# Optimization experiments

Measured on AMD Instinct MI355X. Metric: run time of the kernel, lower is better.

The kernel has to match this reference:

```python
import jax, jax.numpy as jnp
import numpy as np

DIM = 384; HEADS = 6; K = 10; G = 2
GC = DIM // G            # group channel dim
HD = DIM // HEADS        # head dim
SCALE = HD ** -0.5
LN_EPS = 1e-5


def _sqdist(a, b):
    # a: [..., n, 3], b: [..., m, 3] -> [..., n, m]
    return (jnp.sum(a * a, -1)[..., :, None]
            + jnp.sum(b * b, -1)[..., None, :]
            - 2.0 * jnp.einsum('...nc,...mc->...nm', a, b))


def setup_inputs() -> dict:
    key = jax.random.key(0)
    ks = jax.random.split(key, 12)
    B, N, M = 4, 1024, 1024
    s = 0.02
    return {
        'q': jax.random.normal(ks[0], (B, N, DIM), jnp.float32),
        'q_pos': jax.random.normal(ks[1], (B, N, 3), jnp.float32),
        'v': jax.random.normal(ks[2], (B, M, DIM), jnp.float32),
        'v_pos': jax.random.normal(ks[3], (B, M, 3), jnp.float32),
        'Wq': jax.random.normal(ks[4], (DIM, DIM), jnp.float32) * s,
        'Wk': jax.random.normal(ks[5], (DIM, DIM), jnp.float32) * s,
        'Wv': jax.random.normal(ks[6], (DIM, DIM), jnp.float32) * s,
        'Wvoff': jax.random.normal(ks[7], (DIM, DIM), jnp.float32) * s,
        'Woff1': jax.random.normal(ks[8], (DIM, 2 * GC), jnp.float32) * s,
        'boff1': jnp.zeros((DIM,), jnp.float32),
        'ln_g': jnp.ones((DIM,), jnp.float32),
        'ln_b': jnp.zeros((DIM,), jnp.float32),
        'Woff2': jax.random.normal(ks[9], (3, DIM), jnp.float32) * s,
        'Wproj': jax.random.normal(ks[10], (DIM, DIM), jnp.float32) * s,
        'bproj': jnp.zeros((DIM,), jnp.float32),
    }


def reference(q, q_pos, v, v_pos, Wq, Wk, Wv, Wvoff, Woff1, boff1,
              ln_g, ln_b, Woff2, Wproj, bproj):
    B, N, C = q.shape
    M = v.shape[1]

    # --- knn_point: K nearest v_pos for each q_pos ---
    idx = jax.lax.top_k(-_sqdist(q_pos, v_pos), K)[1]        # [B,N,K]
    idx_flat = idx.reshape(B, N * K, 1)

    qp = q @ Wq.T                                            # [B,N,C]
    v_off = v @ Wvoff.T                                      # [B,M,C]

    # index_points gathers
    local_v = jnp.take_along_axis(v_off, idx_flat, axis=1).reshape(B, N, K, C)
    local_v_pos = jnp.take_along_axis(v_pos, idx_flat, axis=1).reshape(B, N, K, 3)

    # group split: 'b n k (g c) -> b g n k c'
    off_local_v = local_v.reshape(B, N, K, G, GC).transpose(0, 3, 1, 2, 4)  # [B,G,N,K,GC]
    group_q = qp.reshape(B, N, G, GC).transpose(0, 2, 1, 3)                 # [B,G,N,GC]

    shift_feat = jnp.concatenate(
        [off_local_v, jnp.broadcast_to(group_q[:, :, :, None, :], (B, G, N, K, GC))], -1)

    # linear_offset MLP: Linear -> LayerNorm -> GELU(exact) -> Linear, then tanh
    h = shift_feat @ Woff1.T + boff1                          # [B,G,N,K,DIM]
    mu = h.mean(-1, keepdims=True)
    var = h.var(-1, keepdims=True)
    h = (h - mu) / jnp.sqrt(var + LN_EPS) * ln_g + ln_b
    h = jax.nn.gelu(h, approximate=False)
    offset = jnp.tanh(h @ Woff2.T)                            # [B,G,N,K,3]

    shift_pos = (local_v_pos[:, None] + offset).reshape(B, G, N * K, 3)
    vg = v.reshape(B, M, G, GC).transpose(0, 2, 1, 3)         # [B,G,M,GC]

    # --- three_nn + reciprocal-distance three_interpolate ---
    sqd = _sqdist(shift_pos, v_pos[:, None])                  # [B,G,N*K,M]
    negd, idx3 = jax.lax.top_k(-sqd, 3)                       # 3 smallest
    dist = jnp.sqrt(jnp.maximum(-negd, 0.0))                  # [B,G,N*K,3]
    w = 1.0 / (dist + 1e-8)
    w = w / jnp.sum(w, -1, keepdims=True)
    feats = jnp.take_along_axis(vg, idx3.reshape(B, G, N * K * 3, 1), axis=2)
    feats = feats.reshape(B, G, N * K, 3, GC)
    interp = jnp.einsum('bgnj,bgnjc->bgnc', w, feats)         # [B,G,N*K,GC]
    # '(b g) (n k) c -> b n k (g c)'
    interp = interp.reshape(B, G, N, K, GC).transpose(0, 2, 3, 1, 4).reshape(B, N, K, C)

    # --- local cross-attention (each query attends to its K interpolated feats) ---
    kf = (interp @ Wk.T).reshape(B, N, K, HEADS, HD)
    vf = (interp @ Wv.T).reshape(B, N, K, HEADS, HD)
    qh = qp.reshape(B, N, HEADS, HD)
    attn = jnp.einsum('bnhd,bnkhd->bhnk', qh, kf) * SCALE
    attn = jax.nn.softmax(attn, axis=-1)
    out = jnp.einsum('bhnk,bnkhd->bnhd', attn, vf).reshape(B, N, C)
    return out @ Wproj.T + bproj
```

## Files before the change

### kernel.cpp

```cpp
#include <hip/hip_runtime.h>
#include <math.h>

#define NB 4
#define NN 1024
#define NM 1024
#define NC 384
#define NK 10
#define NG 2
#define NGC 192
#define NH 6

#define GSZ ((size_t)NB * NM * NC)
#define QSZ ((size_t)NB * NN * NC)
#define NCNC ((size_t)NC * NC)

#define OFF_WQ 0
#define OFF_W1B 147456
#define OFF_WK0 221184
#define OFF_WK1 294912
#define OFF_WV0 368640
#define OFF_WV1 442368
#define OFF_WPROJ 516096
#define WT_ALL_FLOATS 663552

__device__ __forceinline__ float wred_sum(float v) {
#pragma unroll
  for (int m = 32; m >= 1; m >>= 1) v += __shfl_xor(v, m, 64);
  return v;
}

__device__ __forceinline__ ushort f2bf(float x) {
  unsigned u = __float_as_uint(x);
  unsigned r = (u + 0x7fffu + ((u >> 16) & 1u)) >> 16;
  return (ushort)r;
}
__device__ __forceinline__ float b2f(ushort s) {
  return __uint_as_float(((unsigned)s) << 16);
}

__global__ void transpose_all_k(const float* __restrict__ Wq, const float* __restrict__ Woff1,
                                const float* __restrict__ Wk, const float* __restrict__ Wv,
                                const float* __restrict__ Wproj, float* __restrict__ Wt_all) {
  const float* W;
  int i0, icount, doff;
  switch (blockIdx.y) {
    case 0: W = Wq;    i0 = 0;   icount = NC;  doff = OFF_WQ;    break;
    case 1: W = Woff1; i0 = NGC; icount = NGC; doff = OFF_W1B;   break;
    case 2: W = Wk;    i0 = 0;   icount = NGC; doff = OFF_WK0;   break;
    case 3: W = Wk;    i0 = NGC; icount = NGC; doff = OFF_WK1;   break;
    case 4: W = Wv;    i0 = 0;   icount = NGC; doff = OFF_WV0;   break;
    case 5: W = Wv;    i0 = NGC; icount = NGC; doff = OFF_WV1;   break;
    default: W = Wproj; i0 = 0;  icount = NC;  doff = OFF_WPROJ; break;
  }
  int id = blockIdx.x * 256 + threadIdx.x;
  if (id >= icount * NC) return;
  int o = id % NC;
  int i = id / NC;
  Wt_all[doff + (size_t)i * NC + o] = W[(size_t)o * NC + i0 + i];
}

__global__ void wcomb_k(const float* __restrict__ Woff1, const float* __restrict__ Wvoff,
                        float* __restrict__ Wcomb_t) {
  int o = blockIdx.x;
  int g = blockIdx.y;
  int i = threadIdx.x;
  __shared__ float w1[NGC];
  if (i < NGC) w1[i] = Woff1[(size_t)o * NC + i];
  __syncthreads();
  float acc = 0.f;
#pragma unroll 4
  for (int j = 0; j < NGC; ++j)
    acc = fmaf(w1[j], Wvoff[(size_t)(g * NGC + j) * NC + i], acc);
  Wcomb_t[((size_t)g * NC + i) * NC + o] = acc;
}

__global__ __launch_bounds__(384) void gemm16_k(const float* __restrict__ X, int IN, int xoff0,
                                                int xoff_stride, const float* __restrict__ Wt0,
                                                size_t wstride, const float* __restrict__ bias,
                                                float* __restrict__ Y0, size_t ystride) {
  __shared__ __align__(16) float xs[NC][20];
  int tid = threadIdx.x;
  int og = tid % 96, rg = tid / 96;
  int r0 = blockIdx.x * 16;
  int job = blockIdx.y;
  int xoff = xoff0 + job * xoff_stride;
  const float* Wt = Wt0 + (size_t)job * wstride;
  float* Y = Y0 + (size_t)job * ystride;
  for (int t = tid; t < 16 * IN; t += 384) {
    int r = t / IN, kk = t % IN;
    xs[kk][r] = X[(size_t)(r0 + r) * NC + xoff + kk];
  }
  __syncthreads();
  float acc[4][4];
#pragma unroll
  for (int i = 0; i < 4; ++i)
#pragma unroll
    for (int j = 0; j < 4; ++j) acc[i][j] = 0.f;
  int o = og * 4;
#pragma unroll 4
  for (int kk = 0; kk < IN; ++kk) {
    float4 w4 = *(const float4*)&Wt[(size_t)kk * NC + o];
    float4 x4 = *(const float4*)&xs[kk][rg * 4];
    float xr[4] = {x4.x, x4.y, x4.z, x4.w};
    float wr[4] = {w4.x, w4.y, w4.z, w4.w};
#pragma unroll
    for (int ri = 0; ri < 4; ++ri)
#pragma unroll
      for (int oi = 0; oi < 4; ++oi) acc[ri][oi] = fmaf(xr[ri], wr[oi], acc[ri][oi]);
  }
  float4 bv = make_float4(0.f, 0.f, 0.f, 0.f);
  if (bias) bv = *(const float4*)&bias[o];
#pragma unroll
  for (int ri = 0; ri < 4; ++ri) {
    float4 ov;
    ov.x = acc[ri][0] + bv.x;
    ov.y = acc[ri][1] + bv.y;
    ov.z = acc[ri][2] + bv.z;
    ov.w = acc[ri][3] + bv.w;
    *(float4*)&Y[(size_t)(r0 + rg * 4 + ri) * NC + o] = ov;
  }
}

__global__ __launch_bounds__(384) void vproj_k(const float* __restrict__ v,
                                               const float* __restrict__ Wcomb_t,
                                               const float* __restrict__ Wt_all,
                                               float* __restrict__ vcontrib,
                                               ushort* __restrict__ KcT,
                                               ushort* __restrict__ VcT) {
  __shared__ __align__(16) float xs[NC][20];
  int tid = threadIdx.x;
  int og = tid % 96, rg = tid / 96;
  int r0 = blockIdx.x * 16;
  int job = blockIdx.y;
  const float* Wt;
  float* Yf = nullptr;
  ushort* Yh = nullptr;
  int IN, xoff;
  switch (job) {
    case 0: Wt = Wcomb_t;        IN = NC;  xoff = 0;   Yf = vcontrib;       break;
    case 1: Wt = Wcomb_t + NCNC; IN = NC;  xoff = 0;   Yf = vcontrib + GSZ; break;
    case 2: Wt = Wt_all + OFF_WK0; IN = NGC; xoff = 0;   Yh = KcT;          break;
    case 3: Wt = Wt_all + OFF_WK1; IN = NGC; xoff = NGC; Yh = KcT + GSZ;    break;
    case 4: Wt = Wt_all + OFF_WV0; IN = NGC; xoff = 0;   Yh = VcT;          break;
    default: Wt = Wt_all + OFF_WV1; IN = NGC; xoff = NGC; Yh = VcT + GSZ;   break;
  }
  for (int t = tid; t < 16 * IN; t += 384) {
    int r = t / IN, kk = t % IN;
    xs[kk][r] = v[(size_t)(r0 + r) * NC + xoff + kk];
  }
  __syncthreads();
  float acc[4][4];
#pragma unroll
  for (int i = 0; i < 4; ++i)
#pragma unroll
    for (int j = 0; j < 4; ++j) acc[i][j] = 0.f;
  int o = og * 4;
#pragma unroll 4
  for (int kk = 0; kk < IN; ++kk) {
    float4 w4 = *(const float4*)&Wt[(size_t)kk * NC + o];
    float4 x4 = *(const float4*)&xs[kk][rg * 4];
    float xr[4] = {x4.x, x4.y, x4.z, x4.w};
    float wr[4] = {w4.x, w4.y, w4.z, w4.w};
#pragma unroll
    for (int ri = 0; ri < 4; ++ri)
#pragma unroll
      for (int oi = 0; oi < 4; ++oi) acc[ri][oi] = fmaf(xr[ri], wr[oi], acc[ri][oi]);
  }
  if (Yf) {
#pragma unroll
    for (int ri = 0; ri < 4; ++ri)
      *(float4*)&Yf[(size_t)(r0 + rg * 4 + ri) * NC + o] =
          make_float4(acc[ri][0], acc[ri][1], acc[ri][2], acc[ri][3]);
  } else {
#pragma unroll
    for (int ri = 0; ri < 4; ++ri) {
      ushort4 pk;
      pk.x = f2bf(acc[ri][0]);
      pk.y = f2bf(acc[ri][1]);
      pk.z = f2bf(acc[ri][2]);
      pk.w = f2bf(acc[ri][3]);
      *(ushort4*)&Yh[(size_t)(r0 + rg * 4 + ri) * NC + o] = pk;
    }
  }
}

__global__ __launch_bounds__(256) void knn2_k(const float* __restrict__ q_pos,
                                              const float* __restrict__ v_pos,
                                              int* __restrict__ knn_idx) {
  __shared__ float4 cpos[NM];
  int tid = threadIdx.x, lane = tid & 63, wid = tid >> 6;
  int b = blockIdx.x / (NN / 4);
  int n = (blockIdx.x % (NN / 4)) * 4 + wid;
  for (int t = tid; t < NM; t += 256) {
    float x = v_pos[((size_t)b * NM + t) * 3 + 0];
    float y = v_pos[((size_t)b * NM + t) * 3 + 1];
    float z = v_pos[((size_t)b * NM + t) * 3 + 2];
    cpos[t] = make_float4(x, y, z, x * x + y * y + z * z);
  }
  __syncthreads();
  float qx = q_pos[((size_t)b * NN + n) * 3 + 0];
  float qy = q_pos[((size_t)b * NN + n) * 3 + 1];
  float qz = q_pos[((size_t)b * NN + n) * 3 + 2];
  float qq = qx * qx + qy * qy + qz * qz;
  float bd[NK];
  int bi[NK];
#pragma unroll
  for (int j = 0; j < NK; ++j) { bd[j] = 1e30f; bi[j] = 0x7fffffff; }
#pragma unroll
  for (int t = 0; t < NM / 64; ++t) {
    int m = t * 64 + lane;
    float4 cc = cpos[m];
    float d = qq + cc.w - 2.f * (qx * cc.x + qy * cc.y + qz * cc.z);
    if (d < bd[NK - 1]) {
#pragma unroll
      for (int j = NK - 1; j > 0; --j) {
        if (d < bd[j - 1]) { bd[j] = bd[j - 1]; bi[j] = bi[j - 1]; }
        else if (d < bd[j]) { bd[j] = d; bi[j] = m; }
      }
      if (d < bd[0]) { bd[0] = d; bi[0] = m; }
    }
  }
  size_t base = ((size_t)b * NN + n) * NK;
#pragma unroll
  for (int round = 0; round < NK; ++round) {
    float dh = bd[0];
    int mh = bi[0];
#pragma unroll
    for (int off = 32; off >= 1; off >>= 1) {
      float od = __shfl_xor(dh, off, 64);
      int om = __shfl_xor(mh, off, 64);
      if (od < dh || (od == dh && om < mh)) { dh = od; mh = om; }
    }
    if (lane == 0) knn_idx[base + round] = mh;
    if (bi[0] == mh) {
#pragma unroll
      for (int j = 0; j < NK - 1; ++j) { bd[j] = bd[j + 1]; bi[j] = bi[j + 1]; }
      bd[NK - 1] = 1e30f; bi[NK - 1] = 0x7fffffff;
    }
  }
}

__global__ __launch_bounds__(256) void mlp3nn_k(
    const float* __restrict__ vcontrib, const float* __restrict__ qcontrib,
    const float* __restrict__ boff1, const float* __restrict__ ln_g,
    const float* __restrict__ ln_b, const float* __restrict__ Woff2,
    const int* __restrict__ knn_idx, const float* __restrict__ v_pos,
    int* __restrict__ idx3, float* __restrict__ w3) {
  __shared__ float4 cpos[NM];
  int tid = threadIdx.x, lane = tid & 63, wid = tid >> 6;
  int ra = blockIdx.x * 8 + wid * 2;
  int rb = ra + 1;
  int b = (blockIdx.x * 8) / (NK * NN * NG);
  for (int t = tid; t < NM; t += 256) {
    float x = v_pos[((size_t)b * NM + t) * 3 + 0];
    float y = v_pos[((size_t)b * NM + t) * 3 + 1];
    float z = v_pos[((size_t)b * NM + t) * 3 + 2];
    cpos[t] = make_float4(x, y, z, x * x + y * y + z * z);
  }
  __syncthreads();
  int ka = ra % NK, na = (ra / NK) % NN, ga = (ra / (NK * NN)) % NG;
  int kb = rb % NK, nb = (rb / NK) % NN, gb = (rb / (NK * NN)) % NG;
  int ma = knn_idx[((size_t)b * NN + na) * NK + ka];
  int mb = knn_idx[((size_t)b * NN + nb) * NK + kb];
  const float* vca = vcontrib + ((size_t)(ga * NB + b) * NM + ma) * NC;
  const float* qca = qcontrib + ((size_t)(ga * NB + b) * NN + na) * NC;
  const float* vcb = vcontrib + ((size_t)(gb * NB + b) * NM + mb) * NC;
  const float* qcb = qcontrib + ((size_t)(gb * NB + b) * NN + nb) * NC;
  float ha[6], hb[6];
  float sa = 0.f, s2a = 0.f, sb = 0.f, s2b = 0.f;
#pragma unroll
  for (int j = 0; j < 6; ++j) {
    int c = j * 64 + lane;
    float bo = boff1[c];
    float xa = vca[c] + qca[c] + bo;
    float xb = vcb[c] + qcb[c] + bo;
    ha[j] = xa; sa += xa; s2a += xa * xa;
    hb[j] = xb; sb += xb; s2b += xb * xb;
  }
#pragma unroll
  for (int off = 32; off >= 1; off >>= 1) {
    sa += __shfl_xor(sa, off, 64);
    s2a += __shfl_xor(s2a, off, 64);
    sb += __shfl_xor(sb, off, 64);
    s2b += __shfl_xor(s2b, off, 64);
  }
  float meana = sa * (1.f / NC), meanb = sb * (1.f / NC);
  float vara = s2a * (1.f / NC) - meana * meana;
  float varb = s2b * (1.f / NC) - meanb * meanb;
  float inva = 1.f / sqrtf(vara + 1e-5f);
  float invb = 1.f / sqrtf(varb + 1e-5f);
  float p0a = 0.f, p1a = 0.f, p2a = 0.f, p0b = 0.f, p1b = 0.f, p2b = 0.f;
#pragma unroll
  for (int j = 0; j < 6; ++j) {
    int c = j * 64 + lane;
    float gg = ln_g[c], bb = ln_b[c];
    float w0 = Woff2[0 * NC + c], w1 = Woff2[1 * NC + c], w2 = Woff2[2 * NC + c];
    float xa = (ha[j] - meana) * inva * gg + bb;
    xa = 0.5f * xa * (1.f + erff(xa * 0.70710678118654752f));
    float xb = (hb[j] - meanb) * invb * gg + bb;
    xb = 0.5f * xb * (1.f + erff(xb * 0.70710678118654752f));
    p0a = fmaf(xa, w0, p0a); p1a = fmaf(xa, w1, p1a); p2a = fmaf(xa, w2, p2a);
    p0b = fmaf(xb, w0, p0b); p1b = fmaf(xb, w1, p1b); p2b = fmaf(xb, w2, p2b);
  }
#pragma unroll
  for (int off = 32; off >= 1; off >>= 1) {
    p0a += __shfl_xor(p0a, off, 64);
    p1a += __shfl_xor(p1a, off, 64);
    p2a += __shfl_xor(p2a, off, 64);
    p0b += __shfl_xor(p0b, off, 64);
    p1b += __shfl_xor(p1b, off, 64);
    p2b += __shfl_xor(p2b, off, 64);
  }
  float4 cma = cpos[ma], cmb = cpos[mb];
  float sxa = cma.x + tanhf(p0a), sya = cma.y + tanhf(p1a), sza = cma.z + tanhf(p2a);
  float sxb = cmb.x + tanhf(p0b), syb = cmb.y + tanhf(p1b), szb = cmb.z + tanhf(p2b);
  float qqa = sxa * sxa + sya * sya + sza * sza;
  float qqb = sxb * sxb + syb * syb + szb * szb;
  float d0a = 1e30f, d1a = 1e30f, d2a = 1e30f;
  float d0b = 1e30f, d1b = 1e30f, d2b = 1e30f;
  int i0a = 0x7fffffff, i1a = 0x7fffffff, i2a = 0x7fffffff;
  int i0b = 0x7fffffff, i1b = 0x7fffffff, i2b = 0x7fffffff;
#pragma unroll 4
  for (int t = 0; t < NM / 64; ++t) {
    int m2 = t * 64 + lane;
    float4 cc = cpos[m2];
    float da = qqa + cc.w - 2.f * (sxa * cc.x + sya * cc.y + sza * cc.z);
    float db = qqb + cc.w - 2.f * (sxb * cc.x + syb * cc.y + szb * cc.z);
    i2a = (da < d1a) ? i1a : ((da < d2a) ? m2 : i2a);
    d2a = fminf(fmaxf(da, d1a), d2a);
    i1a = (da < d0a) ? i0a : ((da < d1a) ? m2 : i1a);
    d1a = fminf(fmaxf(da, d0a), d1a);
    i0a = (da < d0a) ? m2 : i0a;
    d0a = fminf(da, d0a);
    i2b = (db < d1b) ? i1b : ((db < d2b) ? m2 : i2b);
    d2b = fminf(fmaxf(db, d1b), d2b);
    i1b = (db < d0b) ? i0b : ((db < d1b) ? m2 : i1b);
    d1b = fminf(fmaxf(db, d0b), d1b);
    i0b = (db < d0b) ? m2 : i0b;
    d0b = fminf(db, d0b);
  }
  float rda[3], rdb[3];
  int rma[3], rmb[3];
#pragma unroll
  for (int round = 0; round < 3; ++round) {
    float dha = d0a; int mha = i0a;
    float dhb = d0b; int mhb = i0b;
#pragma unroll
    for (int off = 32; off >= 1; off >>= 1) {
      float oda = __shfl_xor(dha, off, 64); int oma = __shfl_xor(mha, off, 64);
      float odb = __shfl_xor(dhb, off, 64); int omb = __shfl_xor(mhb, off, 64);
      if (oda < dha || (oda == dha && oma < mha)) { dha = oda; mha = oma; }
      if (odb < dhb || (odb == dhb && omb < mhb)) { dhb = odb; mhb = omb; }
    }
    rda[round] = dha; rma[round] = mha;
    rdb[round] = dhb; rmb[round] = mhb;
    if (i0a == mha) { d0a = d1a; i0a = i1a; d1a = d2a; i1a = i2a; d2a = 1e30f; i2a = 0x7fffffff; }
    if (i0b == mhb) { d0b = d1b; i0b = i1b; d1b = d2b; i1b = i2b; d2b = 1e30f; i2b = 0x7fffffff; }
  }
  if (lane == 0) {
    float e0 = 1.f / (sqrtf(fmaxf(rda[0], 0.f)) + 1e-8f);
    float e1 = 1.f / (sqrtf(fmaxf(rda[1], 0.f)) + 1e-8f);
    float e2 = 1.f / (sqrtf(fmaxf(rda[2], 0.f)) + 1e-8f);
    float sw = e0 + e1 + e2;
    idx3[(size_t)ra * 3 + 0] = rma[0]; w3[(size_t)ra * 3 + 0] = e0 / sw;
    idx3[(size_t)ra * 3 + 1] = rma[1]; w3[(size_t)ra * 3 + 1] = e1 / sw;
    idx3[(size_t)ra * 3 + 2] = rma[2]; w3[(size_t)ra * 3 + 2] = e2 / sw;
    float f0 = 1.f / (sqrtf(fmaxf(rdb[0], 0.f)) + 1e-8f);
    float f1 = 1.f / (sqrtf(fmaxf(rdb[1], 0.f)) + 1e-8f);
    float f2 = 1.f / (sqrtf(fmaxf(rdb[2], 0.f)) + 1e-8f);
    float sw2 = f0 + f1 + f2;
    idx3[(size_t)rb * 3 + 0] = rmb[0]; w3[(size_t)rb * 3 + 0] = f0 / sw2;
    idx3[(size_t)rb * 3 + 1] = rmb[1]; w3[(size_t)rb * 3 + 1] = f1 / sw2;
    idx3[(size_t)rb * 3 + 2] = rmb[2]; w3[(size_t)rb * 3 + 2] = f2 / sw2;
  }
}

__global__ __launch_bounds__(NC) void attn_k(const float* __restrict__ qp,
                                             const ushort* __restrict__ Kc,
                                             const ushort* __restrict__ Vc,
                                             const int* __restrict__ idx3,
                                             const float* __restrict__ w3,
                                             float* __restrict__ attn_out) {
  __shared__ float vfs[NK][NC];
  __shared__ float lgs[NH][NK];
  __shared__ int il[NG][NK][3];
  __shared__ float wl[NG][NK][3];
  int o = threadIdx.x;
  int lane = o & 63, wid = o >> 6;
  int b = blockIdx.x / NN;
  int n = blockIdx.x % NN;
  if (o < NG * NK * 3) {
    int g = o / (NK * 3), k = (o / 3) % NK, j = o % 3;
    size_t rr = (((size_t)(b * NG + g) * NN + n) * NK + k) * 3 + j;
    il[g][k][j] = idx3[rr];
    wl[g][k][j] = w3[rr];
  }
  __syncthreads();
  float qv = qp[((size_t)b * NN + n) * NC + o];
  for (int k = 0; k < NK; ++k) {
    float kf = 0.f, vf = 0.f;
#pragma unroll
    for (int g = 0; g < NG; ++g)
#pragma unroll
      for (int j = 0; j < 3; ++j) {
        int m = il[g][k][j];
        float w = wl[g][k][j];
        size_t base = ((size_t)(g * NB + b) * NM + m) * NC + o;
        kf = fmaf(w, b2f(Kc[base]), kf);
        vf = fmaf(w, b2f(Vc[base]), vf);
      }
    vfs[k][o] = vf;
    float p = wred_sum(qv * kf);
    if (lane == 0) lgs[wid][k] = p * 0.125f;
  }
  __syncthreads();
  float a[NK];
  float mx = -1e30f;
#pragma unroll
  for (int k = 0; k < NK; ++k) { a[k] = lgs[wid][k]; mx = fmaxf(mx, a[k]); }
  float sum = 0.f;
#pragma unroll
  for (int k = 0; k < NK; ++k) { a[k] = expf(a[k] - mx); sum += a[k]; }
  float outv = 0.f;
#pragma unroll
  for (int k = 0; k < NK; ++k) outv = fmaf(a[k] / sum, vfs[k][o], outv);
  attn_out[((size_t)b * NN + n) * NC + o] = outv;
}

extern "C" void kernel_launch(void* const* d_in, const int* in_sizes, int n_in,
                              void* d_out, int out_size, void* d_ws, size_t ws_size,
                              hipStream_t stream) {
  (void)in_sizes; (void)n_in; (void)out_size; (void)ws_size;
  const float* q     = (const float*)d_in[0];
  const float* q_pos = (const float*)d_in[1];
  const float* v     = (const float*)d_in[2];
  const float* v_pos = (const float*)d_in[3];
  const float* Wq    = (const float*)d_in[4];
  const float* Wk    = (const float*)d_in[5];
  const float* Wv    = (const float*)d_in[6];
  const float* Wvoff = (const float*)d_in[7];
  const float* Woff1 = (const float*)d_in[8];
  const float* boff1 = (const float*)d_in[9];
  const float* ln_g  = (const float*)d_in[10];
  const float* ln_b  = (const float*)d_in[11];
  const float* Woff2 = (const float*)d_in[12];
  const float* Wproj = (const float*)d_in[13];
  const float* bproj = (const float*)d_in[14];
  float* out = (float*)d_out;

  char* p = (char*)d_ws;
  auto alloc_f = [&](size_t n) { float* r = (float*)p; p += n * sizeof(float); return r; };
  auto alloc_h = [&](size_t n) { ushort* r = (ushort*)p; p += n * sizeof(ushort); return r; };
  auto alloc_i = [&](size_t n) { int* r = (int*)p; p += n * sizeof(int); return r; };

  float* qp        = alloc_f(QSZ);
  float* qcontrib  = alloc_f((size_t)NG * QSZ);
  float* vcontrib  = alloc_f((size_t)NG * GSZ);
  float* Wt_all    = alloc_f((size_t)WT_ALL_FLOATS);
  float* Wcomb_t   = alloc_f((size_t)NG * NCNC);
  float* w3        = alloc_f((size_t)NB * NG * NN * NK * 3);
  ushort* KcT      = alloc_h((size_t)NG * GSZ);
  ushort* VcT      = alloc_h((size_t)NG * GSZ);
  int* knn_idx     = alloc_i((size_t)NB * NN * NK);
  int* idx3        = alloc_i((size_t)NB * NG * NN * NK * 3);
  float* attn_out  = vcontrib;

  transpose_all_k<<<dim3(576, 7), 256, 0, stream>>>(Wq, Woff1, Wk, Wv, Wproj, Wt_all);
  wcomb_k<<<dim3(NC, NG), NC, 0, stream>>>(Woff1, Wvoff, Wcomb_t);

  gemm16_k<<<dim3(NB * NN / 16, 1), 384, 0, stream>>>(q, NC, 0, 0, Wt_all + OFF_WQ, 0, nullptr,
                                                      qp, 0);
  knn2_k<<<NB * (NN / 4), 256, 0, stream>>>(q_pos, v_pos, knn_idx);
  gemm16_k<<<dim3(NB * NN / 16, 2), 384, 0, stream>>>(qp, NGC, 0, NGC, Wt_all + OFF_W1B, 0,
                                                      nullptr, qcontrib, QSZ);
  vproj_k<<<dim3(NB * NM / 16, 6), 384, 0, stream>>>(v, Wcomb_t, Wt_all, vcontrib, KcT, VcT);

  mlp3nn_k<<<NB * NG * NN * NK / 8, 256, 0, stream>>>(vcontrib, qcontrib, boff1, ln_g, ln_b,
                                                      Woff2, knn_idx, v_pos, idx3, w3);
  attn_k<<<NB * NN, NC, 0, stream>>>(qp, KcT, VcT, idx3, w3, attn_out);
  gemm16_k<<<dim3(NB * NN / 16, 1), 384, 0, stream>>>(attn_out, NC, 0, 0, Wt_all + OFF_WPROJ, 0,
                                                      bproj, out, 0);
}
```

Baseline: 476.9 us.

## Interleave bf16 K/V into packed words and fuse K/V projection jobs

K and V projections for each group are now computed in one vproj job that shares the staged input tile and writes a single interleaved buffer of packed bf16 pairs. attn_k then fetches both K and V with one 32-bit load per gathered row instead of two 16-bit loads. mlp3nn_k reuses one q row for its row pair, relying on the two rows always sharing the same n and g. The three-NN insertion uses med3 instructions. The shared-q assumption depends on NK being even so that pairs never straddle a query boundary.

```diff
diff --git a/kernel.cpp b/kernel.cpp
--- a/kernel.cpp
+++ b/kernel.cpp
@@ -34,8 +34,11 @@
   unsigned r = (u + 0x7fffu + ((u >> 16) & 1u)) >> 16;
   return (ushort)r;
 }
-__device__ __forceinline__ float b2f(ushort s) {
-  return __uint_as_float(((unsigned)s) << 16);
+__device__ __forceinline__ float b2f_lo(unsigned kv) {
+  return __uint_as_float(kv << 16);
+}
+__device__ __forceinline__ float b2f_hi(unsigned kv) {
+  return __uint_as_float(kv & 0xffff0000u);
 }
 
 __global__ void transpose_all_k(const float* __restrict__ Wq, const float* __restrict__ Woff1,
@@ -125,61 +128,81 @@
                                                const float* __restrict__ Wcomb_t,
                                                const float* __restrict__ Wt_all,
                                                float* __restrict__ vcontrib,
-                                               ushort* __restrict__ KcT,
-                                               ushort* __restrict__ VcT) {
+                                               unsigned* __restrict__ KVc) {
   __shared__ __align__(16) float xs[NC][20];
   int tid = threadIdx.x;
   int og = tid % 96, rg = tid / 96;
   int r0 = blockIdx.x * 16;
   int job = blockIdx.y;
-  const float* Wt;
-  float* Yf = nullptr;
-  ushort* Yh = nullptr;
-  int IN, xoff;
-  switch (job) {
-    case 0: Wt = Wcomb_t;        IN = NC;  xoff = 0;   Yf = vcontrib;       break;
-    case 1: Wt = Wcomb_t + NCNC; IN = NC;  xoff = 0;   Yf = vcontrib + GSZ; break;
-    case 2: Wt = Wt_all + OFF_WK0; IN = NGC; xoff = 0;   Yh = KcT;          break;
-    case 3: Wt = Wt_all + OFF_WK1; IN = NGC; xoff = NGC; Yh = KcT + GSZ;    break;
-    case 4: Wt = Wt_all + OFF_WV0; IN = NGC; xoff = 0;   Yh = VcT;          break;
-    default: Wt = Wt_all + OFF_WV1; IN = NGC; xoff = NGC; Yh = VcT + GSZ;   break;
-  }
-  for (int t = tid; t < 16 * IN; t += 384) {
-    int r = t / IN, kk = t % IN;
-    xs[kk][r] = v[(size_t)(r0 + r) * NC + xoff + kk];
-  }
-  __syncthreads();
-  float acc[4][4];
-#pragma unroll
-  for (int i = 0; i < 4; ++i)
-#pragma unroll
-    for (int j = 0; j < 4; ++j) acc[i][j] = 0.f;
   int o = og * 4;
+  if (job < 2) {
+    const float* Wt = job ? (Wcomb_t + NCNC) : Wcomb_t;
+    float* Yf = job ? (vcontrib + GSZ) : vcontrib;
+    for (int t = tid; t < 16 * NC; t += 384) {
+      int r = t / NC, kk = t % NC;
+      xs[kk][r] = v[(size_t)(r0 + r) * NC + kk];
+    }
+    __syncthreads();
+    float acc[4][4];
+#pragma unroll
+    for (int i = 0; i < 4; ++i)
+#pragma unroll
+      for (int j = 0; j < 4; ++j) acc[i][j] = 0.f;
 #pragma unroll 4
-  for (int kk = 0; kk < IN; ++kk) {
-    float4 w4 = *(const float4*)&Wt[(size_t)kk * NC + o];
-    float4 x4 = *(const float4*)&xs[kk][rg * 4];
-    float xr[4] = {x4.x, x4.y, x4.z, x4.w};
-    float wr[4] = {w4.x, w4.y, w4.z, w4.w};
-#pragma unroll
-    for (int ri = 0; ri < 4; ++ri)
-#pragma unroll
-      for (int oi = 0; oi < 4; ++oi) acc[ri][oi] = fmaf(xr[ri], wr[oi], acc[ri][oi]);
-  }
-  if (Yf) {
+    for (int kk = 0; kk < NC; ++kk) {
+      float4 w4 = *(const float4*)&Wt[(size_t)kk * NC + o];
+      float4 x4 = *(const float4*)&xs[kk][rg * 4];
+      float xr[4] = {x4.x, x4.y, x4.z, x4.w};
+      float wr[4] = {w4.x, w4.y, w4.z, w4.w};
+#pragma unroll
+      for (int ri = 0; ri < 4; ++ri)
+#pragma unroll
+        for (int oi = 0; oi < 4; ++oi) acc[ri][oi] = fmaf(xr[ri], wr[oi], acc[ri][oi]);
+    }
 #pragma unroll
     for (int ri = 0; ri < 4; ++ri)
       *(float4*)&Yf[(size_t)(r0 + rg * 4 + ri) * NC + o] =
           make_float4(acc[ri][0], acc[ri][1], acc[ri][2], acc[ri][3]);
   } else {
+    int g = job - 2;
+    int xoff = g * NGC;
+    const float* WtK = Wt_all + (g ? OFF_WK1 : OFF_WK0);
+    const float* WtV = Wt_all + (g ? OFF_WV1 : OFF_WV0);
+    unsigned* Yu = KVc + (size_t)g * GSZ;
+    for (int t = tid; t < 16 * NGC; t += 384) {
+      int r = t / NGC, kk = t % NGC;
+      xs[kk][r] = v[(size_t)(r0 + r) * NC + xoff + kk];
+    }
+    __syncthreads();
+    float aK[4][4], aV[4][4];
+#pragma unroll
+    for (int i = 0; i < 4; ++i)
+#pragma unroll
+      for (int j = 0; j < 4; ++j) { aK[i][j] = 0.f; aV[i][j] = 0.f; }
+#pragma unroll 2
+    for (int kk = 0; kk < NGC; ++kk) {
+      float4 wk = *(const float4*)&WtK[(size_t)kk * NC + o];
+      float4 wv = *(const float4*)&WtV[(size_t)kk * NC + o];
+      float4 x4 = *(const float4*)&xs[kk][rg * 4];
+      float xr[4] = {x4.x, x4.y, x4.z, x4.w};
+      float wkr[4] = {wk.x, wk.y, wk.z, wk.w};
+      float wvr[4] = {wv.x, wv.y, wv.z, wv.w};
+#pragma unroll
+      for (int ri = 0; ri < 4; ++ri)
+#pragma unroll
+        for (int oi = 0; oi < 4; ++oi) {
+          aK[ri][oi] = fmaf(xr[ri], wkr[oi], aK[ri][oi]);
+          aV[ri][oi] = fmaf(xr[ri], wvr[oi], aV[ri][oi]);
+        }
+    }
 #pragma unroll
     for (int ri = 0; ri < 4; ++ri) {
-      ushort4 pk;
-      pk.x = f2bf(acc[ri][0]);
-      pk.y = f2bf(acc[ri][1]);
-      pk.z = f2bf(acc[ri][2]);
-      pk.w = f2bf(acc[ri][3]);
-      *(ushort4*)&Yh[(size_t)(r0 + rg * 4 + ri) * NC + o] = pk;
+      uint4 pk;
+      pk.x = (unsigned)f2bf(aK[ri][0]) | ((unsigned)f2bf(aV[ri][0]) << 16);
+      pk.y = (unsigned)f2bf(aK[ri][1]) | ((unsigned)f2bf(aV[ri][1]) << 16);
+      pk.z = (unsigned)f2bf(aK[ri][2]) | ((unsigned)f2bf(aV[ri][2]) << 16);
+      pk.w = (unsigned)f2bf(aK[ri][3]) | ((unsigned)f2bf(aV[ri][3]) << 16);
+      *(uint4*)&Yu[(size_t)(r0 + rg * 4 + ri) * NC + o] = pk;
     }
   }
 }
@@ -258,22 +281,23 @@
     cpos[t] = make_float4(x, y, z, x * x + y * y + z * z);
   }
   __syncthreads();
-  int ka = ra % NK, na = (ra / NK) % NN, ga = (ra / (NK * NN)) % NG;
-  int kb = rb % NK, nb = (rb / NK) % NN, gb = (rb / (NK * NN)) % NG;
+  int ka = ra % NK;
+  int na = (ra / NK) % NN;
+  int ga = (ra / (NK * NN)) % NG;
   int ma = knn_idx[((size_t)b * NN + na) * NK + ka];
-  int mb = knn_idx[((size_t)b * NN + nb) * NK + kb];
+  int mb = knn_idx[((size_t)b * NN + na) * NK + ka + 1];
   const float* vca = vcontrib + ((size_t)(ga * NB + b) * NM + ma) * NC;
+  const float* vcb = vcontrib + ((size_t)(ga * NB + b) * NM + mb) * NC;
   const float* qca = qcontrib + ((size_t)(ga * NB + b) * NN + na) * NC;
-  const float* vcb = vcontrib + ((size_t)(gb * NB + b) * NM + mb) * NC;
-  const float* qcb = qcontrib + ((size_t)(gb * NB + b) * NN + nb) * NC;
   float ha[6], hb[6];
   float sa = 0.f, s2a = 0.f, sb = 0.f, s2b = 0.f;
 #pragma unroll
   for (int j = 0; j < 6; ++j) {
     int c = j * 64 + lane;
+    float qj = qca[c];
     float bo = boff1[c];
-    float xa = vca[c] + qca[c] + bo;
-    float xb = vcb[c] + qcb[c] + bo;
+    float xa = vca[c] + qj + bo;
+    float xb = vcb[c] + qj + bo;
     ha[j] = xa; sa += xa; s2a += xa * xa;
     hb[j] = xb; sb += xb; s2b += xb * xb;
   }
@@ -326,18 +350,20 @@
     float4 cc = cpos[m2];
     float da = qqa + cc.w - 2.f * (sxa * cc.x + sya * cc.y + sza * cc.z);
     float db = qqb + cc.w - 2.f * (sxb * cc.x + syb * cc.y + szb * cc.z);
+    float nd0a = fminf(da, d0a);
+    float nd1a = __builtin_amdgcn_fmed3f(da, d0a, d1a);
+    float nd2a = __builtin_amdgcn_fmed3f(da, d1a, d2a);
     i2a = (da < d1a) ? i1a : ((da < d2a) ? m2 : i2a);
-    d2a = fminf(fmaxf(da, d1a), d2a);
     i1a = (da < d0a) ? i0a : ((da < d1a) ? m2 : i1a);
-    d1a = fminf(fmaxf(da, d0a), d1a);
     i0a = (da < d0a) ? m2 : i0a;
-    d0a = fminf(da, d0a);
+    d0a = nd0a; d1a = nd1a; d2a = nd2a;
+    float nd0b = fminf(db, d0b);
+    float nd1b = __builtin_amdgcn_fmed3f(db, d0b, d1b);
+    float nd2b = __builtin_amdgcn_fmed3f(db, d1b, d2b);
     i2b = (db < d1b) ? i1b : ((db < d2b) ? m2 : i2b);
-    d2b = fminf(fmaxf(db, d1b), d2b);
     i1b = (db < d0b) ? i0b : ((db < d1b) ? m2 : i1b);
-    d1b = fminf(fmaxf(db, d0b), d1b);
     i0b = (db < d0b) ? m2 : i0b;
-    d0b = fminf(db, d0b);
+    d0b = nd0b; d1b = nd1b; d2b = nd2b;
   }
   float rda[3], rdb[3];
   int rma[3], rmb[3];
@@ -376,8 +402,7 @@
 }
 
 __global__ __launch_bounds__(NC) void attn_k(const float* __restrict__ qp,
-                                             const ushort* __restrict__ Kc,
-                                             const ushort* __restrict__ Vc,
+                                             const unsigned* __restrict__ KV,
                                              const int* __restrict__ idx3,
                                              const float* __restrict__ w3,
                                              float* __restrict__ attn_out) {
@@ -405,9 +430,9 @@
       for (int j = 0; j < 3; ++j) {
         int m = il[g][k][j];
         float w = wl[g][k][j];
-        size_t base = ((size_t)(g * NB + b) * NM + m) * NC + o;
-        kf = fmaf(w, b2f(Kc[base]), kf);
-        vf = fmaf(w, b2f(Vc[base]), vf);
+        unsigned kv = KV[((size_t)(g * NB + b) * NM + m) * NC + o];
+        kf = fmaf(w, b2f_lo(kv), kf);
+        vf = fmaf(w, b2f_hi(kv), vf);
       }
     vfs[k][o] = vf;
     float p = wred_sum(qv * kf);
@@ -450,7 +475,7 @@
 
   char* p = (char*)d_ws;
   auto alloc_f = [&](size_t n) { float* r = (float*)p; p += n * sizeof(float); return r; };
-  auto alloc_h = [&](size_t n) { ushort* r = (ushort*)p; p += n * sizeof(ushort); return r; };
+  auto alloc_u = [&](size_t n) { unsigned* r = (unsigned*)p; p += n * sizeof(unsigned); return r; };
   auto alloc_i = [&](size_t n) { int* r = (int*)p; p += n * sizeof(int); return r; };
 
   float* qp        = alloc_f(QSZ);
@@ -459,8 +484,7 @@
   float* Wt_all    = alloc_f((size_t)WT_ALL_FLOATS);
   float* Wcomb_t   = alloc_f((size_t)NG * NCNC);
   float* w3        = alloc_f((size_t)NB * NG * NN * NK * 3);
-  ushort* KcT      = alloc_h((size_t)NG * GSZ);
-  ushort* VcT      = alloc_h((size_t)NG * GSZ);
+  unsigned* KVc    = alloc_u((size_t)NG * GSZ);
   int* knn_idx     = alloc_i((size_t)NB * NN * NK);
   int* idx3        = alloc_i((size_t)NB * NG * NN * NK * 3);
   float* attn_out  = vcontrib;
@@ -473,11 +497,11 @@
   knn2_k<<<NB * (NN / 4), 256, 0, stream>>>(q_pos, v_pos, knn_idx);
   gemm16_k<<<dim3(NB * NN / 16, 2), 384, 0, stream>>>(qp, NGC, 0, NGC, Wt_all + OFF_W1B, 0,
                                                       nullptr, qcontrib, QSZ);
-  vproj_k<<<dim3(NB * NM / 16, 6), 384, 0, stream>>>(v, Wcomb_t, Wt_all, vcontrib, KcT, VcT);
+  vproj_k<<<dim3(NB * NM / 16, 4), 384, 0, stream>>>(v, Wcomb_t, Wt_all, vcontrib, KVc);
 
   mlp3nn_k<<<NB * NG * NN * NK / 8, 256, 0, stream>>>(vcontrib, qcontrib, boff1, ln_g, ln_b,
                                                       Woff2, knn_idx, v_pos, idx3, w3);
-  attn_k<<<NB * NN, NC, 0, stream>>>(qp, KcT, VcT, idx3, w3, attn_out);
+  attn_k<<<NB * NN, NC, 0, stream>>>(qp, KVc, idx3, w3, attn_out);
   gemm16_k<<<dim3(NB * NN / 16, 1), 384, 0, stream>>>(attn_out, NC, 0, 0, Wt_all + OFF_WPROJ, 0,
                                                       bproj, out, 0);
 }
```

Result: faster. 463.2 us (-2.9%).
